# Kernel tuning notes

Hardware: AMD Instinct MI355X
Metric: run time of the kernel (lower is better)

Reference implementation:

```python
import jax, jax.numpy as jnp
import numpy as np

B, S, N, E, H = 64, 32, 64, 128, 4
D = E // H


def setup_inputs() -> dict:
    key = jax.random.key(0)
    ks = jax.random.split(key, 20)
    x = jax.random.normal(ks[0], (B, S, N, E), dtype=jnp.float32)
    adj = jax.random.randint(ks[1], (N, N), 0, 2, dtype=jnp.int32)
    adj = adj.at[jnp.arange(N), jnp.arange(N)].set(1)  # ensure >=1 neighbor per row
    sc = 1.0 / np.sqrt(E)
    def W(k):
        return jax.random.normal(k, (E, E), dtype=jnp.float32) * sc
    inp = {"x": x, "adj": adj}
    names = ["t_Wq", "t_Wk", "t_Wv", "t_Wo", "s_Wq", "s_Wk", "s_Wv", "s_Wo"]
    for i, n in enumerate(names):
        inp[n] = W(ks[2 + i])
        inp[n.replace("W", "b")] = jnp.zeros((E,), dtype=jnp.float32)
    return inp


def reference(x, adj, t_Wq, t_bq, t_Wk, t_bk, t_Wv, t_bv, t_Wo, t_bo,
              s_Wq, s_bq, s_Wk, s_bk, s_Wv, s_bv, s_Wo, s_bo):
    # x: [B,S,N,E]; adj: [N,N]. Queries are the last timestep of each agent.
    b, s, n, e = x.shape
    scale = 1.0 / np.sqrt(D)
    q = x[:, -1]  # [B,N,E]

    # --- temporal attention over each (agent i query, neighbor j sequence) pair ---
    qt = (q @ t_Wq.T + t_bq).reshape(b, n, H, D)            # [B,N,H,D]
    kt = (x @ t_Wk.T + t_bk).reshape(b, s, n, H, D)         # [B,S,M,H,D]
    vt = (x @ t_Wv.T + t_bv).reshape(b, s, n, H, D)
    sc1 = jnp.einsum('bnhd,bsmhd->nmbhs', qt, kt) * scale   # [N,M,B,H,S]
    a1 = jax.nn.softmax(sc1, axis=-1)
    ctx1 = jnp.einsum('nmbhs,bsmhd->nmbhd', a1, vt).reshape(n, n, b, e)
    T = ctx1 @ t_Wo.T + t_bo                                 # [N,M,B,E]

    # --- spatial attention: agent i attends over its neighbors' temporal summaries ---
    # Concatenating only adj[i,j]!=0 neighbors then attending == full attention with
    # a -inf mask on non-neighbors (identical masked softmax).
    qs = (q @ s_Wq.T + s_bq).reshape(b, n, H, D)             # [B,N,H,D]
    ks = (T @ s_Wk.T + s_bk).reshape(n, n, b, H, D)          # [N,M,B,H,D]
    vs = (T @ s_Wv.T + s_bv).reshape(n, n, b, H, D)
    sc2 = jnp.einsum('bnhd,nmbhd->nbhm', qs, ks) * scale     # [N,B,H,M]
    neg = jnp.asarray(-1e9, sc2.dtype)
    mask = (adj > 0)[:, None, None, :]                       # [N,1,1,M]
    sc2 = jnp.where(mask, sc2, neg)
    a2 = jax.nn.softmax(sc2, axis=-1)
    ctx2 = jnp.einsum('nbhm,nmbhd->nbhd', a2, vs).reshape(n, b, e)
    out = ctx2 @ s_Wo.T + s_bo                               # [N,B,E]
    return out.transpose(1, 0, 2)                            # [B,N,E]
```

## Files before the change

### kernel.cpp

```cpp
#include <hip/hip_runtime.h>


constexpr int Bb = 64, Ss = 32, Nn = 64, Ee = 128, Hh = 4, Dd = 32;
constexpr int MS = 2;
constexpr float SCALE = 0.17677669529663687f;

__device__ __forceinline__ float4 f4_load(const float* p) {
  return *reinterpret_cast<const float4*>(p);
}
__device__ __forceinline__ void f4_store(float* p, float4 v) {
  *reinterpret_cast<float4*>(p) = v;
}
__device__ __forceinline__ float dot4(float4 a, float4 b) {
  return a.x * b.x + a.y * b.y + a.z * b.z + a.w * b.w;
}

__global__ __launch_bounds__(128) void fuse_weights_kernel(
    const float* __restrict__ sWk, const float* __restrict__ sbk,
    const float* __restrict__ sWv, const float* __restrict__ sbv,
    const float* __restrict__ tWo, const float* __restrict__ tbo,
    float* __restrict__ Wkp, float* __restrict__ bkp,
    float* __restrict__ Wvp, float* __restrict__ bvp) {
  const int i = blockIdx.x;
  const int which = blockIdx.y;
  const float* sW = which ? sWv : sWk;
  const float* sb = which ? sbv : sbk;
  float* Wp = which ? Wvp : Wkp;
  float* bp = which ? bvp : bkp;
  __shared__ float srow[Ee];
  const int t = threadIdx.x;
  srow[t] = sW[i * Ee + t];
  __syncthreads();
  float acc = 0.f;
  for (int k = 0; k < Ee; ++k) acc += srow[k] * tWo[k * Ee + t];
  Wp[i * Ee + t] = acc;
  if (t == 0) {
    float bb = sb[i];
    for (int k = 0; k < Ee; ++k) bb += srow[k] * tbo[k];
    bp[i] = bb;
  }
}

__global__ __launch_bounds__(256) void qproj_kernel(
    const float* __restrict__ x,
    const float* __restrict__ tWq, const float* __restrict__ tbq,
    const float* __restrict__ sWq, const float* __restrict__ sbq,
    const float* __restrict__ Wkp, const float* __restrict__ bkp,
    float* __restrict__ qt_ws, float* __restrict__ qk2_ws,
    float* __restrict__ qb2_ws) {
  __shared__ float q_l[64 * 132];
  __shared__ float W_l[32 * 128];
  __shared__ float bk_l[128];
  const int b = blockIdx.x;
  const int which = blockIdx.y;
  const float* W = which ? sWq : tWq;
  const float* bias = which ? sbq : tbq;
  const int t = threadIdx.x;
  for (int idx = t; idx < 2048; idx += 256) {
    int nn = idx >> 5, e4 = (idx & 31) << 2;
    f4_store(&q_l[nn * 132 + e4],
             f4_load(&x[(((size_t)b * Ss + (Ss - 1)) * Nn + nn) * Ee + e4]));
  }
  if (which && t < 32) f4_store(&bk_l[t * 4], f4_load(&bkp[t * 4]));

  const int ng = t >> 5;
  const int e0 = (t & 31) << 2;
  float4 acc[8];
#pragma unroll
  for (int j = 0; j < 8; ++j) acc[j] = make_float4(0.f, 0.f, 0.f, 0.f);

  for (int kq = 0; kq < 4; ++kq) {
    __syncthreads();
    for (int idx = t; idx < 1024; idx += 256) {
      int e = idx & 127, k0 = (idx >> 7) << 2;
      float4 w = f4_load(&W[e * Ee + kq * 32 + k0]);
      W_l[(k0 + 0) * 128 + e] = w.x;
      W_l[(k0 + 1) * 128 + e] = w.y;
      W_l[(k0 + 2) * 128 + e] = w.z;
      W_l[(k0 + 3) * 128 + e] = w.w;
    }
    __syncthreads();
#pragma unroll
    for (int j = 0; j < 8; ++j) {
      const int n = ng * 8 + j;
      float4 a = acc[j];
      for (int k0 = 0; k0 < 32; k0 += 4) {
        float4 qv = f4_load(&q_l[n * 132 + kq * 32 + k0]);
        float4 w0 = f4_load(&W_l[(k0 + 0) * 128 + e0]);
        float4 w1 = f4_load(&W_l[(k0 + 1) * 128 + e0]);
        float4 w2 = f4_load(&W_l[(k0 + 2) * 128 + e0]);
        float4 w3 = f4_load(&W_l[(k0 + 3) * 128 + e0]);
        a.x += qv.x * w0.x + qv.y * w1.x + qv.z * w2.x + qv.w * w3.x;
        a.y += qv.x * w0.y + qv.y * w1.y + qv.z * w2.y + qv.w * w3.y;
        a.z += qv.x * w0.z + qv.y * w1.z + qv.z * w2.z + qv.w * w3.z;
        a.w += qv.x * w0.w + qv.y * w1.w + qv.z * w2.w + qv.w * w3.w;
      }
      acc[j] = a;
    }
  }
  float4 bb = f4_load(&bias[e0]);
#pragma unroll
  for (int j = 0; j < 8; ++j) {
    acc[j].x += bb.x; acc[j].y += bb.y; acc[j].z += bb.z; acc[j].w += bb.w;
  }
  if (which == 0) {
#pragma unroll
    for (int j = 0; j < 8; ++j)
      f4_store(&qt_ws[((size_t)b * Nn + ng * 8 + j) * Ee + e0], acc[j]);
    return;
  }
  __syncthreads();
#pragma unroll
  for (int j = 0; j < 8; ++j)
    f4_store(&q_l[(ng * 8 + j) * 132 + e0], acc[j]);
  for (int h = 0; h < 4; ++h) {
    __syncthreads();
    for (int idx = t; idx < 1024; idx += 256) {
      int kk = idx >> 5, e4 = (idx & 31) << 2;
      f4_store(&W_l[kk * 128 + e4], f4_load(&Wkp[(h * 32 + kk) * Ee + e4]));
    }
    __syncthreads();
#pragma unroll
    for (int j = 0; j < 8; ++j) {
      const int n = ng * 8 + j;
      float4 a = make_float4(0.f, 0.f, 0.f, 0.f);
      for (int d0 = 0; d0 < 32; d0 += 4) {
        float4 qv = f4_load(&q_l[n * 132 + h * 32 + d0]);
        float4 w0 = f4_load(&W_l[(d0 + 0) * 128 + e0]);
        float4 w1 = f4_load(&W_l[(d0 + 1) * 128 + e0]);
        float4 w2 = f4_load(&W_l[(d0 + 2) * 128 + e0]);
        float4 w3 = f4_load(&W_l[(d0 + 3) * 128 + e0]);
        a.x += qv.x * w0.x + qv.y * w1.x + qv.z * w2.x + qv.w * w3.x;
        a.y += qv.x * w0.y + qv.y * w1.y + qv.z * w2.y + qv.w * w3.y;
        a.z += qv.x * w0.z + qv.y * w1.z + qv.z * w2.z + qv.w * w3.z;
        a.w += qv.x * w0.w + qv.y * w1.w + qv.z * w2.w + qv.w * w3.w;
      }
      f4_store(&qk2_ws[(((size_t)b * Nn + n) * Hh + h) * Ee + e0], a);
    }
  }
  __syncthreads();
  {
    const int nn = t >> 2, h2 = t & 3;
    float s = 0.f;
    for (int d = 0; d < 32; ++d)
      s += q_l[nn * 132 + h2 * 32 + d] * bk_l[h2 * 32 + d];
    qb2_ws[((size_t)b * Nn + nn) * Hh + h2] = s;
  }
}

__global__ __launch_bounds__(256, 2) void ktvt_kernel(
    const float* __restrict__ x,
    const float* __restrict__ tWk, const float* __restrict__ tbk,
    const float* __restrict__ tWv, const float* __restrict__ tbv,
    float* __restrict__ kt_ws, float* __restrict__ vt_ws) {
  __shared__ float x_l[64 * 132];
  __shared__ float Wk_l[32 * 132];
  __shared__ float Wv_l[32 * 132];
  const int b = blockIdx.x;
  const int s = blockIdx.y;
  const int t = threadIdx.x;
  const int ng = t >> 4;
  const int tx = t & 15;
  const size_t xbase = (((size_t)b * Ss + s) * Nn) * Ee;
  for (int idx = t; idx < 2048; idx += 256) {
    int nn = idx >> 5, e4 = (idx & 31) << 2;
    f4_store(&x_l[nn * 132 + e4], f4_load(&x[xbase + nn * Ee + e4]));
  }
  float4 aK[4][2], aV[4][2];
#pragma unroll
  for (int j = 0; j < 4; ++j)
#pragma unroll
    for (int c = 0; c < 2; ++c) {
      aK[j][c] = make_float4(0.f, 0.f, 0.f, 0.f);
      aV[j][c] = make_float4(0.f, 0.f, 0.f, 0.f);
    }
  for (int kq = 0; kq < 4; ++kq) {
    __syncthreads();
    for (int idx = t; idx < 2048; idx += 256) {
      int which = idx >> 10, i2 = idx & 1023;
      int e = i2 & 127, k0 = (i2 >> 7) << 2;
      const float* Wg = which ? tWv : tWk;
      float* Wl = which ? Wv_l : Wk_l;
      float4 w = f4_load(&Wg[e * Ee + kq * 32 + k0]);
      Wl[(k0 + 0) * 132 + e] = w.x;
      Wl[(k0 + 1) * 132 + e] = w.y;
      Wl[(k0 + 2) * 132 + e] = w.z;
      Wl[(k0 + 3) * 132 + e] = w.w;
    }
    __syncthreads();
#pragma unroll 8
    for (int k = 0; k < 32; ++k) {
      float xv[4];
#pragma unroll
      for (int j = 0; j < 4; ++j)
        xv[j] = x_l[(ng * 4 + j) * 132 + kq * 32 + k];
      float4 wk0 = f4_load(&Wk_l[k * 132 + tx * 4]);
      float4 wk1 = f4_load(&Wk_l[k * 132 + 64 + tx * 4]);
      float4 wv0 = f4_load(&Wv_l[k * 132 + tx * 4]);
      float4 wv1 = f4_load(&Wv_l[k * 132 + 64 + tx * 4]);
#pragma unroll
      for (int j = 0; j < 4; ++j) {
        float a = xv[j];
        aK[j][0].x += a * wk0.x; aK[j][0].y += a * wk0.y;
        aK[j][0].z += a * wk0.z; aK[j][0].w += a * wk0.w;
        aK[j][1].x += a * wk1.x; aK[j][1].y += a * wk1.y;
        aK[j][1].z += a * wk1.z; aK[j][1].w += a * wk1.w;
        aV[j][0].x += a * wv0.x; aV[j][0].y += a * wv0.y;
        aV[j][0].z += a * wv0.z; aV[j][0].w += a * wv0.w;
        aV[j][1].x += a * wv1.x; aV[j][1].y += a * wv1.y;
        aV[j][1].z += a * wv1.z; aV[j][1].w += a * wv1.w;
      }
    }
  }
  float4 bk0 = f4_load(&tbk[tx * 4]);
  float4 bk1 = f4_load(&tbk[64 + tx * 4]);
  float4 bv0 = f4_load(&tbv[tx * 4]);
  float4 bv1 = f4_load(&tbv[64 + tx * 4]);
#pragma unroll
  for (int j = 0; j < 4; ++j) {
    const int n = ng * 4 + j;
    const size_t obase = (((size_t)b * Nn + n) * Ss + s) * Ee;
    float4 o;
    o.x = aK[j][0].x + bk0.x; o.y = aK[j][0].y + bk0.y;
    o.z = aK[j][0].z + bk0.z; o.w = aK[j][0].w + bk0.w;
    f4_store(&kt_ws[obase + tx * 4], o);
    o.x = aK[j][1].x + bk1.x; o.y = aK[j][1].y + bk1.y;
    o.z = aK[j][1].z + bk1.z; o.w = aK[j][1].w + bk1.w;
    f4_store(&kt_ws[obase + 64 + tx * 4], o);
    o.x = aV[j][0].x + bv0.x; o.y = aV[j][0].y + bv0.y;
    o.z = aV[j][0].z + bv0.z; o.w = aV[j][0].w + bv0.w;
    f4_store(&vt_ws[obase + tx * 4], o);
    o.x = aV[j][1].x + bv1.x; o.y = aV[j][1].y + bv1.y;
    o.z = aV[j][1].z + bv1.z; o.w = aV[j][1].w + bv1.w;
    f4_store(&vt_ws[obase + 64 + tx * 4], o);
  }
}

__global__ __launch_bounds__(512, 4) void main_kernel(
    const float* __restrict__ kt_ws, const float* __restrict__ vt_ws,
    const float* __restrict__ qt_ws, const float* __restrict__ qk2_ws,
    const float* __restrict__ qb2_ws, const int* __restrict__ adj,
    float* __restrict__ pctxw, float* __restrict__ pM,
    float* __restrict__ pL) {
  __shared__ float kvK[32 * 132];
  __shared__ float kvV[32 * 132];
  __shared__ float p_l[16 * 4 * 36];
  __shared__ float qt_l[16 * 128];
  __shared__ int adj_l[16 * 64];
  const int b = blockIdx.x;
  const int chunk = blockIdx.y;
  const int ms = chunk >> 2;
  const int n0 = (chunk & 3) * 16;
  const int m0 = ms * 32;
  const int t = threadIdx.x;
  const int n = t >> 5;
  const int lane = t & 31;
  const int e4 = lane << 2;
  const int hh = lane >> 3;

  for (int idx = t; idx < 2048; idx += 512)
    qt_l[idx] = qt_ws[((size_t)b * Nn + n0 + (idx >> 7)) * Ee + (idx & 127)];
  for (int idx = t; idx < 1024; idx += 512)
    adj_l[idx] = adj[(n0 + (idx >> 6)) * Nn + (idx & 63)];

  float4 qk2r[4];
  float qb2r[4];
#pragma unroll
  for (int h = 0; h < 4; ++h) {
    qk2r[h] = f4_load(&qk2_ws[(((size_t)b * Nn + n0 + n) * Hh + h) * Ee + e4]);
    qb2r[h] = qb2_ws[((size_t)b * Nn + n0 + n) * Hh + h];
  }
  float4 cw[4];
  float Mh[4], Lh[4];
#pragma unroll
  for (int h = 0; h < 4; ++h) {
    cw[h] = make_float4(0.f, 0.f, 0.f, 0.f);
    Mh[h] = -1e30f;
    Lh[h] = 0.f;
  }
  __syncthreads();

  for (int mi = 0; mi < 32; ++mi) {
    const int m = m0 + mi;
    const size_t kvbase = ((size_t)b * Nn + m) * Ss * Ee;
#pragma unroll
    for (int p = 0; p < 2; ++p) {
      int idx = p * 512 + t;
      int s = idx >> 5, e = (idx & 31) << 2;
      f4_store(&kvK[s * 132 + e], f4_load(&kt_ws[kvbase + s * Ee + e]));
    }
#pragma unroll
    for (int p = 0; p < 2; ++p) {
      int idx = p * 512 + t;
      int s = idx >> 5, e = (idx & 31) << 2;
      f4_store(&kvV[s * 132 + e], f4_load(&vt_ws[kvbase + s * Ee + e]));
    }
    __syncthreads();
    float pr[4];
#pragma unroll
    for (int h = 0; h < 4; ++h) {
      float a = 0.f;
#pragma unroll
      for (int d0 = 0; d0 < 32; d0 += 4) {
        float4 qa = f4_load(&qt_l[n * 128 + h * 32 + d0]);
        float4 ka = f4_load(&kvK[lane * 132 + h * 32 + d0]);
        a += dot4(qa, ka);
      }
      pr[h] = a * SCALE;
    }
#pragma unroll
    for (int h = 0; h < 4; ++h) {
      float mx = pr[h];
#pragma unroll
      for (int msk = 1; msk < 32; msk <<= 1)
        mx = fmaxf(mx, __shfl_xor(mx, msk));
      float w = __expf(pr[h] - mx);
      float sum = w;
#pragma unroll
      for (int msk = 1; msk < 32; msk <<= 1) sum += __shfl_xor(sum, msk);
      p_l[(n * 4 + h) * 36 + lane] = w * (1.0f / sum);
    }
    __syncthreads();
    float4 c1 = make_float4(0.f, 0.f, 0.f, 0.f);
    const float* prow = &p_l[(n * 4 + hh) * 36];
#pragma unroll
    for (int s4 = 0; s4 < 8; ++s4) {
      float4 pw = f4_load(&prow[s4 * 4]);
      float4 v0 = f4_load(&kvV[(s4 * 4 + 0) * 132 + e4]);
      float4 v1 = f4_load(&kvV[(s4 * 4 + 1) * 132 + e4]);
      float4 v2 = f4_load(&kvV[(s4 * 4 + 2) * 132 + e4]);
      float4 v3 = f4_load(&kvV[(s4 * 4 + 3) * 132 + e4]);
      c1.x += pw.x * v0.x + pw.y * v1.x + pw.z * v2.x + pw.w * v3.x;
      c1.y += pw.x * v0.y + pw.y * v1.y + pw.z * v2.y + pw.w * v3.y;
      c1.z += pw.x * v0.z + pw.y * v1.z + pw.z * v2.z + pw.w * v3.z;
      c1.w += pw.x * v0.w + pw.y * v1.w + pw.z * v2.w + pw.w * v3.w;
    }
    const int am = adj_l[n * 64 + m];
    float s2[4];
#pragma unroll
    for (int h2 = 0; h2 < 4; ++h2) {
      float part = dot4(qk2r[h2], c1);
#pragma unroll
      for (int msk = 1; msk < 32; msk <<= 1) part += __shfl_xor(part, msk);
      s2[h2] = am ? (part + qb2r[h2]) * SCALE : -1e30f;
    }
#pragma unroll
    for (int h2 = 0; h2 < 4; ++h2) {
      float mnew = fmaxf(Mh[h2], s2[h2]);
      float r = __expf(Mh[h2] - mnew);
      float w = (s2[h2] < -1e29f) ? 0.f : __expf(s2[h2] - mnew);
      Lh[h2] = Lh[h2] * r + w;
      cw[h2].x = cw[h2].x * r + w * c1.x;
      cw[h2].y = cw[h2].y * r + w * c1.y;
      cw[h2].z = cw[h2].z * r + w * c1.z;
      cw[h2].w = cw[h2].w * r + w * c1.w;
      Mh[h2] = mnew;
    }
    __syncthreads();
  }
  const size_t pidx = ((size_t)(ms * Bb + b) * Nn + n0 + n);
#pragma unroll
  for (int h2 = 0; h2 < 4; ++h2)
    f4_store(&pctxw[(pidx * 4 + h2) * Ee + e4], cw[h2]);
  if (lane == 0) {
#pragma unroll
    for (int h2 = 0; h2 < 4; ++h2) {
      pM[pidx * 4 + h2] = Mh[h2];
      pL[pidx * 4 + h2] = Lh[h2];
    }
  }
}

__global__ __launch_bounds__(256) void reduce_kernel(
    const float* __restrict__ pctxw, const float* __restrict__ pM,
    const float* __restrict__ pL, const float* __restrict__ Wvp,
    const float* __restrict__ bvp, const float* __restrict__ sWo,
    const float* __restrict__ sbo, float* __restrict__ out) {
  __shared__ float cwf[8 * 4 * 132];
  __shared__ float c2l[8 * 132];
  const int b = blockIdx.x;
  const int n0 = blockIdx.y * 8;
  const int t = threadIdx.x;
  const int n = t >> 5;
  const int lane = t & 31;
  const int e4 = lane << 2;
  const int gn = n0 + n;
#pragma unroll
  for (int h = 0; h < 4; ++h) {
    const size_t i0 = ((size_t)(0 * Bb + b) * Nn + gn) * 4 + h;
    const size_t i1 = ((size_t)(1 * Bb + b) * Nn + gn) * 4 + h;
    float M0 = pM[i0], M1 = pM[i1];
    float L0 = pL[i0], L1 = pL[i1];
    float Msx = fmaxf(M0, M1);
    float r0 = __expf(M0 - Msx), r1 = __expf(M1 - Msx);
    float inv = 1.0f / (r0 * L0 + r1 * L1);
    float4 c0 = f4_load(&pctxw[i0 * Ee + e4]);
    float4 c1 = f4_load(&pctxw[i1 * Ee + e4]);
    float4 res;
    res.x = (r0 * c0.x + r1 * c1.x) * inv;
    res.y = (r0 * c0.y + r1 * c1.y) * inv;
    res.z = (r0 * c0.z + r1 * c1.z) * inv;
    res.w = (r0 * c0.w + r1 * c1.w) * inv;
    f4_store(&cwf[(n * 4 + h) * 132 + e4], res);
  }
  __syncthreads();
  {
    const int k4 = lane << 2;
    const int h = lane >> 3;
    float4 a = f4_load(&bvp[k4]);
    for (int ee = 0; ee < 128; ee += 4) {
      float4 cv = f4_load(&cwf[(n * 4 + h) * 132 + ee]);
      float4 w0 = f4_load(&Wvp[(k4 + 0) * Ee + ee]);
      float4 w1 = f4_load(&Wvp[(k4 + 1) * Ee + ee]);
      float4 w2 = f4_load(&Wvp[(k4 + 2) * Ee + ee]);
      float4 w3 = f4_load(&Wvp[(k4 + 3) * Ee + ee]);
      a.x += dot4(w0, cv);
      a.y += dot4(w1, cv);
      a.z += dot4(w2, cv);
      a.w += dot4(w3, cv);
    }
    f4_store(&c2l[n * 132 + k4], a);
  }
  __syncthreads();
  {
    float4 o = f4_load(&sbo[e4]);
    for (int k0 = 0; k0 < 128; k0 += 4) {
      float4 cv = f4_load(&c2l[n * 132 + k0]);
      float4 w0 = f4_load(&sWo[(e4 + 0) * Ee + k0]);
      float4 w1 = f4_load(&sWo[(e4 + 1) * Ee + k0]);
      float4 w2 = f4_load(&sWo[(e4 + 2) * Ee + k0]);
      float4 w3 = f4_load(&sWo[(e4 + 3) * Ee + k0]);
      o.x += dot4(w0, cv);
      o.y += dot4(w1, cv);
      o.z += dot4(w2, cv);
      o.w += dot4(w3, cv);
    }
    f4_store(&out[((size_t)b * Nn + gn) * Ee + e4], o);
  }
}

extern "C" void kernel_launch(void* const* d_in, const int* in_sizes, int n_in,
                              void* d_out, int out_size, void* d_ws,
                              size_t ws_size, hipStream_t stream) {
  const float* x = (const float*)d_in[0];
  const int* adj = (const int*)d_in[1];
  const float* tWq = (const float*)d_in[2];
  const float* tbq = (const float*)d_in[3];
  const float* tWk = (const float*)d_in[4];
  const float* tbk = (const float*)d_in[5];
  const float* tWv = (const float*)d_in[6];
  const float* tbv = (const float*)d_in[7];
  const float* tWo = (const float*)d_in[8];
  const float* tbo = (const float*)d_in[9];
  const float* sWq = (const float*)d_in[10];
  const float* sbq = (const float*)d_in[11];
  const float* sWk = (const float*)d_in[12];
  const float* sbk = (const float*)d_in[13];
  const float* sWv = (const float*)d_in[14];
  const float* sbv = (const float*)d_in[15];
  const float* sWo = (const float*)d_in[16];
  const float* sbo = (const float*)d_in[17];
  float* out = (float*)d_out;

  float* ws = (float*)d_ws;
  const size_t ktvt_elems = (size_t)Bb * Nn * Ss * Ee;
  float* kt_ws = ws;
  float* vt_ws = kt_ws + ktvt_elems;
  float* qt_ws = vt_ws + ktvt_elems;
  float* qk2_ws = qt_ws + (size_t)Bb * Nn * Ee;
  float* qb2_ws = qk2_ws + (size_t)Bb * Nn * Hh * Ee;
  float* Wkp = qb2_ws + (size_t)Bb * Nn * Hh;
  float* Wvp = Wkp + Ee * Ee;
  float* bkp = Wvp + Ee * Ee;
  float* bvp = bkp + Ee;
  float* pctxw = bvp + Ee;
  float* pM = pctxw + (size_t)MS * Bb * Nn * 4 * Ee;
  float* pL = pM + (size_t)MS * Bb * Nn * 4;

  fuse_weights_kernel<<<dim3(Ee, 2), 128, 0, stream>>>(
      sWk, sbk, sWv, sbv, tWo, tbo, Wkp, bkp, Wvp, bvp);
  qproj_kernel<<<dim3(Bb, 2), 256, 0, stream>>>(
      x, tWq, tbq, sWq, sbq, Wkp, bkp, qt_ws, qk2_ws, qb2_ws);
  ktvt_kernel<<<dim3(Bb, Ss), 256, 0, stream>>>(x, tWk, tbk, tWv, tbv, kt_ws,
                                                vt_ws);
  main_kernel<<<dim3(Bb, 8), 512, 0, stream>>>(
      kt_ws, vt_ws, qt_ws, qk2_ws, qb2_ws, adj, pctxw, pM, pL);
  reduce_kernel<<<dim3(Bb, 8), 256, 0, stream>>>(pctxw, pM, pL, Wvp, bvp, sWo,
                                                 sbo, out);
}
```

Baseline: 589.4 us.

## Remap main kernel to 64-lane wavefronts, skip non-neighbors, shrink ktvt smem

Main kernel now gives each 64-lane wavefront one query agent and 8 agents per block, with twice as many blocks. The two half-waves split the heads for scores and the timesteps for the context, then combine with a cross-half shuffle. Non-adjacent neighbors skip the temporal attention entirely, which removes work for the masked entries. The ktvt kernel halves its weight tile in shared memory and raises the occupancy hint so more blocks fit per CU. The cost is more K/V tile reloads across blocks, since each block now reuses each tile for only 8 queries instead of 16.

Result: slower. 1.047 ms (+77.6%).

```diff
diff --git a/kernel.cpp b/kernel.cpp
--- a/kernel.cpp
+++ b/kernel.cpp
@@ -148,14 +148,14 @@
   }
 }
 
-__global__ __launch_bounds__(256, 2) void ktvt_kernel(
+__global__ __launch_bounds__(256, 3) void ktvt_kernel(
     const float* __restrict__ x,
     const float* __restrict__ tWk, const float* __restrict__ tbk,
     const float* __restrict__ tWv, const float* __restrict__ tbv,
     float* __restrict__ kt_ws, float* __restrict__ vt_ws) {
   __shared__ float x_l[64 * 132];
-  __shared__ float Wk_l[32 * 132];
-  __shared__ float Wv_l[32 * 132];
+  __shared__ float Wk_l[16 * 132];
+  __shared__ float Wv_l[16 * 132];
   const int b = blockIdx.x;
   const int s = blockIdx.y;
   const int t = threadIdx.x;
@@ -174,26 +174,26 @@
       aK[j][c] = make_float4(0.f, 0.f, 0.f, 0.f);
       aV[j][c] = make_float4(0.f, 0.f, 0.f, 0.f);
     }
-  for (int kq = 0; kq < 4; ++kq) {
-    __syncthreads();
-    for (int idx = t; idx < 2048; idx += 256) {
-      int which = idx >> 10, i2 = idx & 1023;
+  for (int kc = 0; kc < 8; ++kc) {
+    __syncthreads();
+    for (int idx = t; idx < 1024; idx += 256) {
+      int which = idx >> 9, i2 = idx & 511;
       int e = i2 & 127, k0 = (i2 >> 7) << 2;
       const float* Wg = which ? tWv : tWk;
       float* Wl = which ? Wv_l : Wk_l;
-      float4 w = f4_load(&Wg[e * Ee + kq * 32 + k0]);
+      float4 w = f4_load(&Wg[e * Ee + kc * 16 + k0]);
       Wl[(k0 + 0) * 132 + e] = w.x;
       Wl[(k0 + 1) * 132 + e] = w.y;
       Wl[(k0 + 2) * 132 + e] = w.z;
       Wl[(k0 + 3) * 132 + e] = w.w;
     }
     __syncthreads();
-#pragma unroll 8
-    for (int k = 0; k < 32; ++k) {
+#pragma unroll
+    for (int k = 0; k < 16; ++k) {
       float xv[4];
 #pragma unroll
       for (int j = 0; j < 4; ++j)
-        xv[j] = x_l[(ng * 4 + j) * 132 + kq * 32 + k];
+        xv[j] = x_l[(ng * 4 + j) * 132 + kc * 16 + k];
       float4 wk0 = f4_load(&Wk_l[k * 132 + tx * 4]);
       float4 wk1 = f4_load(&Wk_l[k * 132 + 64 + tx * 4]);
       float4 wv0 = f4_load(&Wv_l[k * 132 + tx * 4]);
@@ -236,7 +236,7 @@
   }
 }
 
-__global__ __launch_bounds__(512, 4) void main_kernel(
+__global__ __launch_bounds__(512, 6) void main_kernel(
     const float* __restrict__ kt_ws, const float* __restrict__ vt_ws,
     const float* __restrict__ qt_ws, const float* __restrict__ qk2_ws,
     const float* __restrict__ qb2_ws, const int* __restrict__ adj,
@@ -244,31 +244,37 @@
     float* __restrict__ pL) {
   __shared__ float kvK[32 * 132];
   __shared__ float kvV[32 * 132];
-  __shared__ float p_l[16 * 4 * 36];
-  __shared__ float qt_l[16 * 128];
-  __shared__ int adj_l[16 * 64];
+  __shared__ float p_l[32 * 36];
+  __shared__ float qt_l[8 * 128];
+  __shared__ int adj_l[8 * 64];
   const int b = blockIdx.x;
   const int chunk = blockIdx.y;
-  const int ms = chunk >> 2;
-  const int n0 = (chunk & 3) * 16;
+  const int ms = chunk >> 3;
+  const int n0 = (chunk & 7) * 8;
   const int m0 = ms * 32;
   const int t = threadIdx.x;
-  const int n = t >> 5;
-  const int lane = t & 31;
-  const int e4 = lane << 2;
-  const int hh = lane >> 3;
-
-  for (int idx = t; idx < 2048; idx += 512)
-    qt_l[idx] = qt_ws[((size_t)b * Nn + n0 + (idx >> 7)) * Ee + (idx & 127)];
-  for (int idx = t; idx < 1024; idx += 512)
-    adj_l[idx] = adj[(n0 + (idx >> 6)) * Nn + (idx & 63)];
+  const int w = t >> 6;
+  const int l64 = t & 63;
+  const int gn = n0 + w;
+  const int sc_s = l64 & 31;
+  const int sc_h0 = (l64 >> 5) * 2;
+  const int sh = l64 >> 5;
+  const int eidx = l64 & 31;
+  const int e4 = eidx << 2;
+  const int ph = eidx >> 3;
+
+  for (int idx = t; idx < 256; idx += 512)
+    f4_store(&qt_l[idx * 4],
+             f4_load(&qt_ws[((size_t)b * Nn + n0 + (idx >> 5)) * Ee +
+                            ((idx & 31) << 2)]));
+  if (t < 512) adj_l[t] = adj[(n0 + (t >> 6)) * Nn + (t & 63)];
 
   float4 qk2r[4];
   float qb2r[4];
 #pragma unroll
   for (int h = 0; h < 4; ++h) {
-    qk2r[h] = f4_load(&qk2_ws[(((size_t)b * Nn + n0 + n) * Hh + h) * Ee + e4]);
-    qb2r[h] = qb2_ws[((size_t)b * Nn + n0 + n) * Hh + h];
+    qk2r[h] = f4_load(&qk2_ws[(((size_t)b * Nn + gn) * Hh + h) * Ee + e4]);
+    qb2r[h] = qb2_ws[((size_t)b * Nn + gn) * Hh + h];
   }
   float4 cw[4];
   float Mh[4], Lh[4];
@@ -296,77 +302,83 @@
       f4_store(&kvV[s * 132 + e], f4_load(&vt_ws[kvbase + s * Ee + e]));
     }
     __syncthreads();
-    float pr[4];
-#pragma unroll
-    for (int h = 0; h < 4; ++h) {
-      float a = 0.f;
-#pragma unroll
-      for (int d0 = 0; d0 < 32; d0 += 4) {
-        float4 qa = f4_load(&qt_l[n * 128 + h * 32 + d0]);
-        float4 ka = f4_load(&kvK[lane * 132 + h * 32 + d0]);
-        a += dot4(qa, ka);
-      }
-      pr[h] = a * SCALE;
-    }
-#pragma unroll
-    for (int h = 0; h < 4; ++h) {
-      float mx = pr[h];
-#pragma unroll
-      for (int msk = 1; msk < 32; msk <<= 1)
-        mx = fmaxf(mx, __shfl_xor(mx, msk));
-      float w = __expf(pr[h] - mx);
-      float sum = w;
-#pragma unroll
-      for (int msk = 1; msk < 32; msk <<= 1) sum += __shfl_xor(sum, msk);
-      p_l[(n * 4 + h) * 36 + lane] = w * (1.0f / sum);
-    }
-    __syncthreads();
-    float4 c1 = make_float4(0.f, 0.f, 0.f, 0.f);
-    const float* prow = &p_l[(n * 4 + hh) * 36];
-#pragma unroll
-    for (int s4 = 0; s4 < 8; ++s4) {
-      float4 pw = f4_load(&prow[s4 * 4]);
-      float4 v0 = f4_load(&kvV[(s4 * 4 + 0) * 132 + e4]);
-      float4 v1 = f4_load(&kvV[(s4 * 4 + 1) * 132 + e4]);
-      float4 v2 = f4_load(&kvV[(s4 * 4 + 2) * 132 + e4]);
-      float4 v3 = f4_load(&kvV[(s4 * 4 + 3) * 132 + e4]);
-      c1.x += pw.x * v0.x + pw.y * v1.x + pw.z * v2.x + pw.w * v3.x;
-      c1.y += pw.x * v0.y + pw.y * v1.y + pw.z * v2.y + pw.w * v3.y;
-      c1.z += pw.x * v0.z + pw.y * v1.z + pw.z * v2.z + pw.w * v3.z;
-      c1.w += pw.x * v0.w + pw.y * v1.w + pw.z * v2.w + pw.w * v3.w;
-    }
-    const int am = adj_l[n * 64 + m];
-    float s2[4];
-#pragma unroll
-    for (int h2 = 0; h2 < 4; ++h2) {
-      float part = dot4(qk2r[h2], c1);
-#pragma unroll
-      for (int msk = 1; msk < 32; msk <<= 1) part += __shfl_xor(part, msk);
-      s2[h2] = am ? (part + qb2r[h2]) * SCALE : -1e30f;
-    }
-#pragma unroll
-    for (int h2 = 0; h2 < 4; ++h2) {
-      float mnew = fmaxf(Mh[h2], s2[h2]);
-      float r = __expf(Mh[h2] - mnew);
-      float w = (s2[h2] < -1e29f) ? 0.f : __expf(s2[h2] - mnew);
-      Lh[h2] = Lh[h2] * r + w;
-      cw[h2].x = cw[h2].x * r + w * c1.x;
-      cw[h2].y = cw[h2].y * r + w * c1.y;
-      cw[h2].z = cw[h2].z * r + w * c1.z;
-      cw[h2].w = cw[h2].w * r + w * c1.w;
-      Mh[h2] = mnew;
-    }
-    __syncthreads();
-  }
-  const size_t pidx = ((size_t)(ms * Bb + b) * Nn + n0 + n);
-#pragma unroll
-  for (int h2 = 0; h2 < 4; ++h2)
-    f4_store(&pctxw[(pidx * 4 + h2) * Ee + e4], cw[h2]);
-  if (lane == 0) {
-#pragma unroll
-    for (int h2 = 0; h2 < 4; ++h2) {
-      pM[pidx * 4 + h2] = Mh[h2];
-      pL[pidx * 4 + h2] = Lh[h2];
+    const int am = adj_l[w * 64 + m];
+    if (am) {
+#pragma unroll
+      for (int j = 0; j < 2; ++j) {
+        const int h = sc_h0 + j;
+        float a = 0.f;
+#pragma unroll
+        for (int d0 = 0; d0 < 32; d0 += 4)
+          a += dot4(f4_load(&qt_l[w * 128 + h * 32 + d0]),
+                    f4_load(&kvK[sc_s * 132 + h * 32 + d0]));
+        a *= SCALE;
+        float mx = a;
+#pragma unroll
+        for (int msk = 1; msk < 32; msk <<= 1)
+          mx = fmaxf(mx, __shfl_xor(mx, msk));
+        float ww = __expf(a - mx);
+        float sum = ww;
+#pragma unroll
+        for (int msk = 1; msk < 32; msk <<= 1) sum += __shfl_xor(sum, msk);
+        p_l[(w * 4 + h) * 36 + sc_s] = ww * (1.0f / sum);
+      }
+    }
+    __syncthreads();
+    if (am) {
+      float4 c1 = make_float4(0.f, 0.f, 0.f, 0.f);
+      const float* prow = &p_l[(w * 4 + ph) * 36 + sh * 16];
+#pragma unroll
+      for (int s4 = 0; s4 < 4; ++s4) {
+        float4 pw = f4_load(&prow[s4 * 4]);
+        const int sb = sh * 16 + s4 * 4;
+        float4 v0 = f4_load(&kvV[(sb + 0) * 132 + e4]);
+        float4 v1 = f4_load(&kvV[(sb + 1) * 132 + e4]);
+        float4 v2 = f4_load(&kvV[(sb + 2) * 132 + e4]);
+        float4 v3 = f4_load(&kvV[(sb + 3) * 132 + e4]);
+        c1.x += pw.x * v0.x + pw.y * v1.x + pw.z * v2.x + pw.w * v3.x;
+        c1.y += pw.x * v0.y + pw.y * v1.y + pw.z * v2.y + pw.w * v3.y;
+        c1.z += pw.x * v0.z + pw.y * v1.z + pw.z * v2.z + pw.w * v3.z;
+        c1.w += pw.x * v0.w + pw.y * v1.w + pw.z * v2.w + pw.w * v3.w;
+      }
+      c1.x += __shfl_xor(c1.x, 32);
+      c1.y += __shfl_xor(c1.y, 32);
+      c1.z += __shfl_xor(c1.z, 32);
+      c1.w += __shfl_xor(c1.w, 32);
+      float s2[4];
+#pragma unroll
+      for (int h2 = 0; h2 < 4; ++h2) {
+        float part = dot4(qk2r[h2], c1);
+#pragma unroll
+        for (int msk = 1; msk < 32; msk <<= 1) part += __shfl_xor(part, msk);
+        s2[h2] = (part + qb2r[h2]) * SCALE;
+      }
+#pragma unroll
+      for (int h2 = 0; h2 < 4; ++h2) {
+        float mnew = fmaxf(Mh[h2], s2[h2]);
+        float r = __expf(Mh[h2] - mnew);
+        float ww = __expf(s2[h2] - mnew);
+        Lh[h2] = Lh[h2] * r + ww;
+        cw[h2].x = cw[h2].x * r + ww * c1.x;
+        cw[h2].y = cw[h2].y * r + ww * c1.y;
+        cw[h2].z = cw[h2].z * r + ww * c1.z;
+        cw[h2].w = cw[h2].w * r + ww * c1.w;
+        Mh[h2] = mnew;
+      }
+    }
+    __syncthreads();
+  }
+  const size_t pidx = ((size_t)(ms * Bb + b) * Nn + gn);
+  if (l64 < 32) {
+#pragma unroll
+    for (int h2 = 0; h2 < 4; ++h2)
+      f4_store(&pctxw[(pidx * 4 + h2) * Ee + e4], cw[h2]);
+    if (l64 == 0) {
+#pragma unroll
+      for (int h2 = 0; h2 < 4; ++h2) {
+        pM[pidx * 4 + h2] = Mh[h2];
+        pL[pidx * 4 + h2] = Lh[h2];
+      }
     }
   }
 }
@@ -483,7 +495,7 @@
       x, tWq, tbq, sWq, sbq, Wkp, bkp, qt_ws, qk2_ws, qb2_ws);
   ktvt_kernel<<<dim3(Bb, Ss), 256, 0, stream>>>(x, tWk, tbk, tWv, tbv, kt_ws,
                                                 vt_ws);
-  main_kernel<<<dim3(Bb, 8), 512, 0, stream>>>(
+  main_kernel<<<dim3(Bb, 16), 512, 0, stream>>>(
       kt_ws, vt_ws, qt_ws, qk2_ws, qb2_ws, adj, pctxw, pM, pL);
   reduce_kernel<<<dim3(Bb, 8), 256, 0, stream>>>(pctxw, pM, pL, Wvp, bvp, sWo,
                                                  sbo, out);
```
